# Kernel tuning notes

Hardware: AMD Instinct MI355X
Metric: run time of the kernel (lower is better)

The kernel has to match this reference:

```python
import jax, jax.numpy as jnp
import numpy as np

B = 32          # graphs per batch
NPG = 2048      # nodes per graph
N = B * NPG     # 65536 total nodes
EPG = 16384     # edges per graph
E = B * EPG     # 524288 total edges
F_IN = 129
H, C = 4, 64    # heads, per-head channels
HC = H * C      # 256
NEG_SLOPE = 0.2 # GATConv LeakyReLU slope


def setup_inputs() -> dict:
    key = jax.random.key(0)
    ks = jax.random.split(key, 20)
    # node features
    x = jax.random.normal(ks[0], (N, F_IN), dtype=jnp.float32)
    # random edges, endpoints within the same graph (per-graph contiguous node ids)
    off = (jnp.arange(B) * NPG)[:, None]
    src = (jax.random.randint(ks[1], (B, EPG), 0, NPG) + off).reshape(-1)
    dst = (jax.random.randint(ks[2], (B, EPG), 0, NPG) + off).reshape(-1)
    edge_index = jnp.stack([src, dst]).astype(jnp.int64)

    def lin(k, fan_in, shape):
        return jax.random.normal(k, shape, dtype=jnp.float32) / np.sqrt(fan_in)

    return {
        "x": x,
        "edge_index": edge_index,
        "lin0_w": lin(ks[3], F_IN, (F_IN, 256)),
        "lin0_b": jnp.zeros((256,), jnp.float32),
        "gat0_W": lin(ks[4], 256, (256, HC)),
        "gat0_asrc": lin(ks[5], C, (H, C)),
        "gat0_adst": lin(ks[6], C, (H, C)),
        "gat0_b": jnp.zeros((HC,), jnp.float32),
        "pool0_w": lin(ks[7], HC, (HC,)),
        "gat1_W": lin(ks[8], HC, (HC, HC)),
        "gat1_asrc": lin(ks[9], C, (H, C)),
        "gat1_adst": lin(ks[10], C, (H, C)),
        "gat1_b": jnp.zeros((HC,), jnp.float32),
        "pool1_w": lin(ks[11], HC, (HC,)),
        "gate_w": lin(ks[12], HC, (HC, 1)),
        "gate_b": jnp.zeros((1,), jnp.float32),
    }


def _leaky(z):
    return jnp.where(z > 0, z, NEG_SLOPE * z)


def _gat(h_in, src, dst, emask, W, asrc, adst, b):
    """PyG GATConv: shared lin, edge attention, segment softmax over dest, self-loops, concat heads."""
    n = h_in.shape[0]
    h = (h_in @ W).reshape(n, H, C)                       # [n,H,C]
    loops = jnp.arange(n)
    s = jnp.concatenate([src, loops])                     # add self loops
    d = jnp.concatenate([dst, loops])
    m = jnp.concatenate([emask, jnp.ones((n,), bool)])
    a_s = jnp.einsum('nhc,hc->nh', h, asrc)               # [n,H]
    a_d = jnp.einsum('nhc,hc->nh', h, adst)
    logit = _leaky(a_s[s] + a_d[d])                       # [E+n,H]
    logit = jnp.where(m[:, None], logit, -1e9)
    mx = jax.ops.segment_max(logit, d, num_segments=n)    # stable segment softmax
    ex = jnp.exp(logit - mx[d]) * m[:, None].astype(logit.dtype)
    den = jax.ops.segment_sum(ex, d, num_segments=n)
    coef = ex / (den[d] + 1e-16)                          # [E+n,H]
    out = jax.ops.segment_sum(h[s] * coef[:, :, None], d, num_segments=n)
    return out.reshape(n, HC) + b


def _topk_pool(hx, src, dst, emask, w, n_in, k):
    """PyG TopKPooling: score = x.w/||w||, per-graph top-k, x' = x[perm]*tanh(score[perm]), edge filter+reindex."""
    n_tot = hx.shape[0]
    bb = n_tot // n_in
    score = (hx @ w) / (jnp.linalg.norm(w) + 1e-16)       # [n_tot]
    _, idx = jax.lax.top_k(score.reshape(bb, n_in), k)    # [bb,k]
    perm = (idx + (jnp.arange(bb) * n_in)[:, None]).reshape(-1)
    xs = hx[perm] * jnp.tanh(score[perm])[:, None]
    newid = jnp.full((n_tot,), -1, jnp.int32).at[perm].set(jnp.arange(bb * k, dtype=jnp.int32))
    ns, nd = newid[src], newid[dst]
    valid = emask & (ns >= 0) & (nd >= 0)
    ns = jnp.where(valid, ns, 0)
    nd = jnp.where(valid, nd, 0)
    return xs, ns, nd, valid


def _attpool(hx, n, gate_w, gate_b):
    """AttentionalAggregation: softmax(gate_nn(x)) per graph, weighted sum."""
    bb = hx.shape[0] // n
    gate = (hx @ gate_w + gate_b).reshape(bb, n)
    wts = jax.nn.softmax(gate, axis=1)
    return jnp.einsum('bn,bnf->bf', wts, hx.reshape(bb, n, -1))


def reference(x, edge_index, lin0_w, lin0_b, gat0_W, gat0_asrc, gat0_adst, gat0_b,
              pool0_w, gat1_W, gat1_asrc, gat1_adst, gat1_b, pool1_w, gate_w, gate_b):
    src, dst = edge_index[0], edge_index[1]
    emask = jnp.ones((E,), bool)
    h = jax.nn.relu(x @ lin0_w + lin0_b)                                  # hidden MLP
    h = jax.nn.elu(_gat(h, src, dst, emask, gat0_W, gat0_asrc, gat0_adst, gat0_b))
    h, src, dst, emask = _topk_pool(h, src, dst, emask, pool0_w, NPG, NPG // 2)
    out = _attpool(h, NPG // 2, gate_w, gate_b)                           # [B,256]
    h = jax.nn.elu(_gat(h, src, dst, emask, gat1_W, gat1_asrc, gat1_adst, gat1_b))
    h, src, dst, emask = _topk_pool(h, src, dst, emask, pool1_w, NPG // 2, NPG // 4)
    out = out + _attpool(h, NPG // 4, gate_w, gate_b)
    return out
```

## Files before the change

### kernel.cpp

```cpp
#include <hip/hip_runtime.h>
#include <cmath>

namespace {

constexpr int NN0 = 65536;
constexpr int NB  = 32;
constexpr int NE  = 524288;
constexpr int EPG = 16384;
constexpr int FIN = 129;
constexpr int KP  = 160;

typedef short bf16x8 __attribute__((ext_vector_type(8)));
typedef float f32x4 __attribute__((ext_vector_type(4)));

__device__ inline float leakyrelu(float z) { return z > 0.f ? z : 0.2f * z; }
__device__ inline float eluf(float z) { return z > 0.f ? z : expm1f(z); }

__device__ inline unsigned short f2bf(float x) {
  union { float f; unsigned int u; } v; v.f = x;
  unsigned int r = v.u + 0x7fffu + ((v.u >> 16) & 1u);
  return (unsigned short)(r >> 16);
}
__device__ inline float bf2f(unsigned short h) {
  union { unsigned int u; float f; } v; v.u = ((unsigned int)h) << 16;
  return v.f;
}

__device__ inline float4 f4fma(float4 a, float c, float4 acc) {
  acc.x += a.x * c; acc.y += a.y * c; acc.z += a.z * c; acc.w += a.w * c;
  return acc;
}

__device__ inline int swz_block(int bid, int bpgl) {
  int x = bid & 7;
  int local = bid >> 3;
  int g = x + ((local >> bpgl) << 3);
  return (g << bpgl) + (local & ((1 << bpgl) - 1));
}

__device__ __forceinline__ void gload_lds16(const unsigned short* g, unsigned short* l) {
  __builtin_amdgcn_global_load_lds((const unsigned int*)g, (unsigned int*)l, 16, 0, 0);
}

__device__ inline void pack_w_body(const float* __restrict__ W, int Kreal, int idx,
                                   unsigned short* __restrict__ hi,
                                   unsigned short* __restrict__ lo) {
  int j = idx & 7;
  int lane = (idx >> 3) & 63;
  int ct = (idx >> 9) & 15;
  int kt = idx >> 13;
  int k = kt * 32 + ((lane >> 4) << 3) + j;
  int c = ct * 16 + (lane & 15);
  float v = (k < Kreal) ? W[(size_t)k * 256 + c] : 0.f;
  unsigned short h = f2bf(v);
  hi[idx] = h;
  lo[idx] = f2bf(v - bf2f(h));
}

__global__ __launch_bounds__(1024) void prep(
    const float* __restrict__ x,
    const float* __restrict__ w0, const float* __restrict__ w1,
    const float* __restrict__ w2,
    const float* __restrict__ pw0, const float* __restrict__ pw1,
    const int* __restrict__ src, const int* __restrict__ dst,
    unsigned short* __restrict__ xhi, unsigned short* __restrict__ xlo,
    unsigned short* __restrict__ whi0, unsigned short* __restrict__ wlo0,
    unsigned short* __restrict__ whi1, unsigned short* __restrict__ wlo1,
    unsigned short* __restrict__ whi2, unsigned short* __restrict__ wlo2,
    float* __restrict__ norms, int* __restrict__ newid,
    int* __restrict__ cursor, int* __restrict__ csr) {
  __shared__ int cnt[2048];
  const int NX = NN0 * KP / 8192;
  const int NW0 = 5 * 8192 / 1024;
  const int NW = 8 * 8192 / 1024;
  const int NC = NN0 / 1024;
  int b = blockIdx.x, tid = threadIdx.x;
  if (b < NX) {
    const int base = (b * 1024 + tid) * 8;
    const int row = base / KP;
    const int c0 = base - row * KP;
    const float* xr = &x[(size_t)row * FIN];
    bf16x8 hv, lv;
#pragma unroll
    for (int i = 0; i < 8; i++) {
      const int c = c0 + i;
      float v = (c < FIN) ? xr[c] : 0.f;
      unsigned short h = f2bf(v);
      hv[i] = (short)h;
      lv[i] = (short)f2bf(v - bf2f(h));
    }
    *reinterpret_cast<bf16x8*>(&xhi[base]) = hv;
    *reinterpret_cast<bf16x8*>(&xlo[base]) = lv;
    return;
  }
  b -= NX;
  if (b < NW0) { pack_w_body(w0, FIN, b * 1024 + tid, whi0, wlo0); return; }
  b -= NW0;
  if (b < NW) { pack_w_body(w1, 256, b * 1024 + tid, whi1, wlo1); return; }
  b -= NW;
  if (b < NW) { pack_w_body(w2, 256, b * 1024 + tid, whi2, wlo2); return; }
  b -= NW;
  if (b < NC) {
    newid[b * 1024 + tid] = -1;
    return;
  }
  b -= NC;
  if (b < NB) {
    const int g = b;
    cnt[tid] = 0;
    cnt[tid + 1024] = 0;
    __syncthreads();
    const int e0 = g * EPG;
    for (int i = tid; i < EPG; i += 1024) {
      int e = e0 + i;
      int d = dst[e];
      int pos = atomicAdd(&cnt[d - (g << 11)], 1);
      if (pos < 64) csr[(size_t)d * 64 + pos] = src[e];
    }
    __syncthreads();
    cursor[(g << 11) + tid] = cnt[tid];
    cursor[(g << 11) + tid + 1024] = cnt[tid + 1024];
    return;
  }
  if (tid < 64) {
    float a0 = 0.f, a1 = 0.f;
#pragma unroll
    for (int j = tid; j < 256; j += 64) {
      float v0 = pw0[j]; a0 += v0 * v0;
      float v1 = pw1[j]; a1 += v1 * v1;
    }
#pragma unroll
    for (int off = 32; off >= 1; off >>= 1) {
      a0 += __shfl_xor(a0, off);
      a1 += __shfl_xor(a1, off);
    }
    if (tid == 0) {
      norms[0] = 1.f / (sqrtf(a0) + 1e-16f);
      norms[1] = 1.f / (sqrtf(a1) + 1e-16f);
    }
  }
}

__global__ __launch_bounds__(256, 2) void gemm_fused(
    const unsigned short* __restrict__ Xhi, const unsigned short* __restrict__ Xlo,
    const unsigned short* __restrict__ B0hi, const unsigned short* __restrict__ B0lo,
    const float* __restrict__ bias0,
    const unsigned short* __restrict__ B1hi, const unsigned short* __restrict__ B1lo,
    float* __restrict__ Out,
    const float* __restrict__ attsrc, const float* __restrict__ attdst,
    float* __restrict__ a_s, float* __restrict__ a_d) {
  __shared__ __align__(16) unsigned short As[2][2][64][32];
  __shared__ __align__(16) char Hsh[2][64 * 512];
  const int tid = threadIdx.x;
  const int lane = tid & 63;
  const int w = tid >> 6;
  const int row0 = blockIdx.x * 64;
  const int l15 = lane & 15, q = lane >> 4;
  const int srow16 = lane >> 2;
  const int skc = (lane & 3) * 8;

  auto stage = [&](int nb, int kt) {
    const size_t goff = (size_t)(row0 + w * 16 + srow16) * KP + kt * 32 + skc;
    gload_lds16(Xhi + goff, &As[nb][0][w * 16][0]);
    gload_lds16(Xlo + goff, &As[nb][1][w * 16][0]);
  };

  f32x4 acc[4][4];
#pragma unroll
  for (int mf = 0; mf < 4; mf++)
#pragma unroll
    for (int nf = 0; nf < 4; nf++) acc[mf][nf] = (f32x4)(0.f);

  stage(0, 0);
  __syncthreads();

#pragma unroll
  for (int kt = 0; kt < 5; ++kt) {
    const int nb = kt & 1;
    if (kt + 1 < 5) stage(nb ^ 1, kt + 1);
    bf16x8 bh[4], bl[4];
#pragma unroll
    for (int nf = 0; nf < 4; nf++) {
      const int ct = w * 4 + nf;
      const size_t bbase = ((size_t)((kt * 16 + ct) * 64 + lane)) << 3;
      bh[nf] = *reinterpret_cast<const bf16x8*>(B0hi + bbase);
      bl[nf] = *reinterpret_cast<const bf16x8*>(B0lo + bbase);
    }
#pragma unroll
    for (int mf = 0; mf < 4; mf++) {
      const int ar = mf * 16 + l15;
      bf16x8 ah = *reinterpret_cast<const bf16x8*>(&As[nb][0][ar][q * 8]);
      bf16x8 al = *reinterpret_cast<const bf16x8*>(&As[nb][1][ar][q * 8]);
#pragma unroll
      for (int nf = 0; nf < 4; nf++) {
        acc[mf][nf] = __builtin_amdgcn_mfma_f32_16x16x32_bf16(ah, bh[nf], acc[mf][nf], 0, 0, 0);
        acc[mf][nf] = __builtin_amdgcn_mfma_f32_16x16x32_bf16(ah, bl[nf], acc[mf][nf], 0, 0, 0);
        acc[mf][nf] = __builtin_amdgcn_mfma_f32_16x16x32_bf16(al, bh[nf], acc[mf][nf], 0, 0, 0);
      }
    }
    __syncthreads();
  }

#pragma unroll
  for (int mf = 0; mf < 4; mf++) {
#pragma unroll
    for (int r = 0; r < 4; r++) {
      const int row = mf * 16 + q * 4 + r;
#pragma unroll
      for (int nf = 0; nf < 4; nf++) {
        const int col = w * 64 + nf * 16 + l15;
        float v = acc[mf][nf][r] + bias0[col];
        v = fmaxf(v, 0.f);
        unsigned short h = f2bf(v);
        unsigned short l = f2bf(v - bf2f(h));
        unsigned int off = (unsigned int)(row * 512 + col * 2) ^ ((row & 7) << 4);
        *reinterpret_cast<unsigned short*>(&Hsh[0][off]) = h;
        *reinterpret_cast<unsigned short*>(&Hsh[1][off]) = l;
        acc[mf][nf][r] = 0.f;
      }
    }
  }
  __syncthreads();

#pragma unroll
  for (int kt = 0; kt < 8; ++kt) {
    bf16x8 bh[4], bl[4];
#pragma unroll
    for (int nf = 0; nf < 4; nf++) {
      const int ct = w * 4 + nf;
      const size_t bbase = ((size_t)((kt * 16 + ct) * 64 + lane)) << 3;
      bh[nf] = *reinterpret_cast<const bf16x8*>(B1hi + bbase);
      bl[nf] = *reinterpret_cast<const bf16x8*>(B1lo + bbase);
    }
#pragma unroll
    for (int mf = 0; mf < 4; mf++) {
      const int ar = mf * 16 + l15;
      unsigned int off = (unsigned int)(ar * 512 + kt * 64 + q * 16) ^ ((ar & 7) << 4);
      bf16x8 ah = *reinterpret_cast<const bf16x8*>(&Hsh[0][off]);
      bf16x8 al = *reinterpret_cast<const bf16x8*>(&Hsh[1][off]);
#pragma unroll
      for (int nf = 0; nf < 4; nf++) {
        acc[mf][nf] = __builtin_amdgcn_mfma_f32_16x16x32_bf16(ah, bh[nf], acc[mf][nf], 0, 0, 0);
        acc[mf][nf] = __builtin_amdgcn_mfma_f32_16x16x32_bf16(ah, bl[nf], acc[mf][nf], 0, 0, 0);
        acc[mf][nf] = __builtin_amdgcn_mfma_f32_16x16x32_bf16(al, bh[nf], acc[mf][nf], 0, 0, 0);
      }
    }
  }

#pragma unroll
  for (int mf = 0; mf < 4; mf++) {
    const int rowb = row0 + mf * 16 + q * 4;
#pragma unroll
    for (int r = 0; r < 4; r++) {
#pragma unroll
      for (int nf = 0; nf < 4; nf++) {
        const int col = w * 64 + nf * 16 + l15;
        Out[(size_t)(rowb + r) * 256 + col] = acc[mf][nf][r];
      }
    }
  }
  const int head = w;
  float sv[4], dv[4];
#pragma unroll
  for (int nf = 0; nf < 4; nf++) {
    sv[nf] = attsrc[head * 64 + nf * 16 + l15];
    dv[nf] = attdst[head * 64 + nf * 16 + l15];
  }
#pragma unroll
  for (int mf = 0; mf < 4; mf++) {
#pragma unroll
    for (int r = 0; r < 4; r++) {
      float ps = 0.f, pd = 0.f;
#pragma unroll
      for (int nf = 0; nf < 4; nf++) {
        ps += acc[mf][nf][r] * sv[nf];
        pd += acc[mf][nf][r] * dv[nf];
      }
#pragma unroll
      for (int off = 8; off >= 1; off >>= 1) {
        ps += __shfl_xor(ps, off);
        pd += __shfl_xor(pd, off);
      }
      if (l15 == 0) {
        const int row = row0 + mf * 16 + q * 4 + r;
        a_s[(size_t)row * 4 + head] = ps;
        a_d[(size_t)row * 4 + head] = pd;
      }
    }
  }
}

template <int KT, bool INDIR>
__global__ __launch_bounds__(256, 2) void gemm_mfma(
    const unsigned short* __restrict__ Xhi, const unsigned short* __restrict__ Xlo,
    int ldx,
    const unsigned short* __restrict__ Bhi, const unsigned short* __restrict__ Blo,
    float* __restrict__ Out,
    const float* __restrict__ attsrc, const float* __restrict__ attdst,
    float* __restrict__ a_s, float* __restrict__ a_d,
    const int* __restrict__ rowmap, const float* __restrict__ tscale, int swzl,
    int ngemm, const float* __restrict__ partials, float* __restrict__ outp,
    int nch) {
  __shared__ __align__(16) unsigned short As[2][2][128][32];
  const int tid = threadIdx.x;
  if ((int)blockIdx.x >= ngemm) {
    int g = blockIdx.x - ngemm, c = tid;
    float a = 0.f;
    for (int s = 0; s < nch; s++) a += partials[((size_t)g * nch + s) * 256 + c];
    outp[g * 256 + c] = a;
    return;
  }
  const int lane = tid & 63;
  const int w = tid >> 6;
  const int rb = (swzl >= 0) ? swz_block(blockIdx.x, swzl) : blockIdx.x;
  const int row0 = rb * 128;
  const int l15 = lane & 15, q = lane >> 4;
  const int sl4 = lane >> 2;
  const int skc = (lane & 3) * 8;

  size_t gr[2];
#pragma unroll
  for (int i = 0; i < 2; i++) {
    int lr = row0 + (w + 4 * i) * 16 + sl4;
    gr[i] = INDIR ? (size_t)rowmap[lr] : (size_t)lr;
  }

  auto stage = [&](int nb, int kt) {
#pragma unroll
    for (int i = 0; i < 2; i++) {
      const int rbase = (w + 4 * i) * 16;
      const size_t goff = gr[i] * ldx + kt * 32 + skc;
      gload_lds16(Xhi + goff, &As[nb][0][rbase][0]);
      gload_lds16(Xlo + goff, &As[nb][1][rbase][0]);
    }
  };

  f32x4 acc[8][4];
#pragma unroll
  for (int mf = 0; mf < 8; mf++)
#pragma unroll
    for (int nf = 0; nf < 4; nf++) acc[mf][nf] = (f32x4)(0.f);

  stage(0, 0);
  __syncthreads();

#pragma unroll
  for (int kt = 0; kt < KT; ++kt) {
    const int nb = kt & 1;
    if (kt + 1 < KT) stage(nb ^ 1, kt + 1);
    bf16x8 bh[4], bl[4];
#pragma unroll
    for (int nf = 0; nf < 4; nf++) {
      const int ct = w * 4 + nf;
      const size_t bbase = ((size_t)((kt * 16 + ct) * 64 + lane)) << 3;
      bh[nf] = *reinterpret_cast<const bf16x8*>(Bhi + bbase);
      bl[nf] = *reinterpret_cast<const bf16x8*>(Blo + bbase);
    }
#pragma unroll
    for (int mf = 0; mf < 8; mf++) {
      const int ar = mf * 16 + l15;
      bf16x8 ah = *reinterpret_cast<const bf16x8*>(&As[nb][0][ar][q * 8]);
      bf16x8 al = *reinterpret_cast<const bf16x8*>(&As[nb][1][ar][q * 8]);
#pragma unroll
      for (int nf = 0; nf < 4; nf++) {
        acc[mf][nf] = __builtin_amdgcn_mfma_f32_16x16x32_bf16(ah, bh[nf], acc[mf][nf], 0, 0, 0);
        acc[mf][nf] = __builtin_amdgcn_mfma_f32_16x16x32_bf16(ah, bl[nf], acc[mf][nf], 0, 0, 0);
        acc[mf][nf] = __builtin_amdgcn_mfma_f32_16x16x32_bf16(al, bh[nf], acc[mf][nf], 0, 0, 0);
      }
    }
    __syncthreads();
  }

#pragma unroll
  for (int mf = 0; mf < 8; mf++) {
    const int rowb = row0 + mf * 16 + q * 4;
#pragma unroll
    for (int r = 0; r < 4; r++) {
      const float ts = INDIR ? tscale[rowb + r] : 1.f;
#pragma unroll
      for (int nf = 0; nf < 4; nf++) {
        float v = acc[mf][nf][r];
        if constexpr (INDIR) v *= ts;
        const int col = w * 64 + nf * 16 + l15;
        Out[(size_t)(rowb + r) * 256 + col] = v;
      }
    }
  }
  const int head = w;
  float sv[4], dv[4];
#pragma unroll
  for (int nf = 0; nf < 4; nf++) {
    sv[nf] = attsrc[head * 64 + nf * 16 + l15];
    dv[nf] = attdst[head * 64 + nf * 16 + l15];
  }
#pragma unroll
  for (int mf = 0; mf < 8; mf++) {
#pragma unroll
    for (int r = 0; r < 4; r++) {
      float ps = 0.f, pd = 0.f;
#pragma unroll
      for (int nf = 0; nf < 4; nf++) {
        ps += acc[mf][nf][r] * sv[nf];
        pd += acc[mf][nf][r] * dv[nf];
      }
#pragma unroll
      for (int off = 8; off >= 1; off >>= 1) {
        ps += __shfl_xor(ps, off);
        pd += __shfl_xor(pd, off);
      }
      if (l15 == 0) {
        const int row = row0 + mf * 16 + q * 4 + r;
        float ts = INDIR ? tscale[row] : 1.f;
        a_s[(size_t)row * 4 + head] = ps * ts;
        a_d[(size_t)row * 4 + head] = pd * ts;
      }
    }
  }
}

__global__ __launch_bounds__(256) void gat_node8(
    const int* __restrict__ cursor, const int* __restrict__ csr,
    const float* __restrict__ a_s, const float* __restrict__ a_d,
    const float* __restrict__ hW, const float* __restrict__ bias,
    const float* __restrict__ pool_w, const float* __restrict__ inv_norm,
    const float* __restrict__ gate_w,
    unsigned short* __restrict__ outHi, unsigned short* __restrict__ outLo,
    float* __restrict__ score, float* __restrict__ graw, int bpgl) {
  const int lane = threadIdx.x & 63;
  const int wv = threadIdx.x >> 6;
  const int dbase = swz_block(blockIdx.x, bpgl) * 8 + wv * 2;
  const int g = lane >> 4, l16 = lane & 15;
  const int d = dbase + (g >> 1);
  const int h0 = (g & 1) * 2;

  const int deg = min(cursor[d], 63);
  const int dim = deg + 1;

  int dmaxw = dim;
  dmaxw = max(dmaxw, __shfl_xor(dmaxw, 32));
  const int nch = (dmaxw + 15) >> 4;

  const float2 ad2 = *reinterpret_cast<const float2*>(&a_d[(size_t)d * 4 + h0]);

  int sreg[4];
  float L0[4], L1[4];
#pragma unroll
  for (int c = 0; c < 4; c++) {
    if (c < nch) {
      const int j = c * 16 + l16;
      const bool has = j < dim;
      int s = (j < deg) ? csr[(size_t)d * 64 + j] : d;
      sreg[c] = s;
      float2 as2 = *reinterpret_cast<const float2*>(&a_s[(size_t)s * 4 + h0]);
      L0[c] = has ? leakyrelu(as2.x + ad2.x) : -1e30f;
      L1[c] = has ? leakyrelu(as2.y + ad2.y) : -1e30f;
    } else {
      sreg[c] = d;
      L0[c] = -1e30f; L1[c] = -1e30f;
    }
  }
  float m0 = fmaxf(fmaxf(L0[0], L0[1]), fmaxf(L0[2], L0[3]));
  float m1 = fmaxf(fmaxf(L1[0], L1[1]), fmaxf(L1[2], L1[3]));
#pragma unroll
  for (int off = 1; off <= 8; off <<= 1) {
    m0 = fmaxf(m0, __shfl_xor(m0, off));
    m1 = fmaxf(m1, __shfl_xor(m1, off));
  }
  float e0[4], e1[4];
  float dn0 = 0.f, dn1 = 0.f;
#pragma unroll
  for (int c = 0; c < 4; c++) {
    if (c < nch) {
      e0[c] = __expf(L0[c] - m0);
      e1[c] = __expf(L1[c] - m1);
      dn0 += e0[c]; dn1 += e1[c];
    } else {
      e0[c] = 0.f; e1[c] = 0.f;
    }
  }
#pragma unroll
  for (int off = 1; off <= 8; off <<= 1) {
    dn0 += __shfl_xor(dn0, off);
    dn1 += __shfl_xor(dn1, off);
  }

  float4 acc0 = {0.f, 0.f, 0.f, 0.f}, acc1 = {0.f, 0.f, 0.f, 0.f};
#pragma unroll
  for (int c = 0; c < 4; c++) {
    if (c < nch) {
      const int tmax = min(16, dmaxw - c * 16);
#pragma unroll 2
      for (int tt = 0; tt < tmax; tt++) {
        const int idx = g * 16 + tt;
        int st = __shfl(sreg[c], idx);
        float c0 = __shfl(e0[c], idx), c1 = __shfl(e1[c], idx);
        if (c * 16 + tt < dim) {
          const float4* hp = reinterpret_cast<const float4*>(&hW[(size_t)st * 256]) + l16;
          acc0 = f4fma(hp[h0 * 16],       c0, acc0);
          acc1 = f4fma(hp[(h0 + 1) * 16], c1, acc1);
        }
      }
    }
  }

  const float iv0 = 1.f / (dn0 + 1e-16f), iv1 = 1.f / (dn1 + 1e-16f);
  float sd = 0.f, gd = 0.f;
#pragma unroll
  for (int h = 0; h < 2; h++) {
    const int coff = (h0 + h) * 64 + l16 * 4;
    float4 vb = h ? acc1 : acc0;
    float iv = h ? iv1 : iv0;
    float4 bb = *reinterpret_cast<const float4*>(&bias[coff]);
    float4 o;
    o.x = eluf(vb.x * iv + bb.x);
    o.y = eluf(vb.y * iv + bb.y);
    o.z = eluf(vb.z * iv + bb.z);
    o.w = eluf(vb.w * iv + bb.w);
    ushort4 oh, ol;
    oh.x = f2bf(o.x); ol.x = f2bf(o.x - bf2f(oh.x));
    oh.y = f2bf(o.y); ol.y = f2bf(o.y - bf2f(oh.y));
    oh.z = f2bf(o.z); ol.z = f2bf(o.z - bf2f(oh.z));
    oh.w = f2bf(o.w); ol.w = f2bf(o.w - bf2f(oh.w));
    *reinterpret_cast<ushort4*>(&outHi[(size_t)d * 256 + coff]) = oh;
    *reinterpret_cast<ushort4*>(&outLo[(size_t)d * 256 + coff]) = ol;
    float4 pw = *reinterpret_cast<const float4*>(&pool_w[coff]);
    float4 gw = *reinterpret_cast<const float4*>(&gate_w[coff]);
    sd += o.x * pw.x + o.y * pw.y + o.z * pw.z + o.w * pw.w;
    gd += o.x * gw.x + o.y * gw.y + o.z * gw.z + o.w * gw.w;
  }
#pragma unroll
  for (int off = 1; off <= 16; off <<= 1) {
    sd += __shfl_xor(sd, off);
    gd += __shfl_xor(gd, off);
  }
  if ((lane & 31) == 0) {
    score[d] = sd * inv_norm[0];
    graw[d] = gd;
  }
}

__global__ __launch_bounds__(1024) void topk_hsel(
    const float* __restrict__ score, const float* __restrict__ graw,
    const float* __restrict__ gate_b, int npg, int k,
    int* __restrict__ perm, int* __restrict__ newid,
    float* __restrict__ gate, float* __restrict__ tsc) {
  __shared__ unsigned keys[2048];
  __shared__ int hist[1024];
  __shared__ int ssum[1024];
  __shared__ int segtot[16];
  __shared__ unsigned wmin[16], wmax[16];
  __shared__ int sstate[3];
  __shared__ int scnt;
  __shared__ int candi[512];
  __shared__ unsigned candk[512];
  __shared__ float fred[1024];
  const int g = blockIdx.x, tid = threadIdx.x;
  const int wv = tid >> 6, ln = tid & 63;
  const size_t base = (size_t)g * npg;

  unsigned mymin = 0xFFFFFFFFu, mymax = 0u;
  for (int i = tid; i < npg; i += 1024) {
    unsigned u = __float_as_uint(score[base + i]);
    u = (u & 0x80000000u) ? ~u : (u | 0x80000000u);
    keys[i] = u;
    mymin = min(mymin, u);
    mymax = max(mymax, u);
  }
#pragma unroll
  for (int off = 32; off >= 1; off >>= 1) {
    mymin = min(mymin, (unsigned)__shfl_xor((int)mymin, off));
    mymax = max(mymax, (unsigned)__shfl_xor((int)mymax, off));
  }
  if (ln == 0) { wmin[wv] = mymin; wmax[wv] = mymax; }
  __syncthreads();
  unsigned lo, hi;
  {
    unsigned a = 0xFFFFFFFFu, b = 0u;
#pragma unroll
    for (int i = 0; i < 16; i++) { a = min(a, wmin[i]); b = max(b, wmax[i]); }
    lo = a; hi = b;
  }
  int need = k;

  for (int iter = 0; iter < 4; ++iter) {
    unsigned long long range = (unsigned long long)(hi - lo) + 1ull;
    unsigned width = (unsigned)((range + 1023ull) >> 10);
    hist[tid] = 0;
    __syncthreads();
    for (int i = tid; i < npg; i += 1024) {
      unsigned u = keys[i];
      if (u >= lo && u <= hi) atomicAdd(&hist[(u - lo) / width], 1);
    }
    __syncthreads();
    int v = hist[tid];
    int s = v;
#pragma unroll
    for (int off = 1; off < 64; off <<= 1) {
      int t = __shfl_down(s, off);
      if (ln + off < 64) s += t;
    }
    if (ln == 0) segtot[wv] = s;
    __syncthreads();
    if (tid == 0) {
      int acc = 0;
      for (int i = 15; i >= 0; i--) { int t = segtot[i]; segtot[i] = acc; acc += t; }
    }
    __syncthreads();
    int S = s + segtot[wv];
    ssum[tid] = S;
    __syncthreads();
    int gt = (tid == 1023) ? 0 : ssum[tid + 1];
    if (S >= need && gt < need) {
      sstate[0] = tid;
      sstate[1] = gt;
      sstate[2] = hist[tid];
    }
    __syncthreads();
    const int bstar = sstate[0], cntAbove = sstate[1], m = sstate[2];
    unsigned nlo = lo + (unsigned)bstar * width;
    unsigned long long nhiu = (unsigned long long)lo + (unsigned long long)(bstar + 1) * width - 1ull;
    unsigned nhi = (nhiu > (unsigned long long)hi) ? hi : (unsigned)nhiu;
    need -= cntAbove;
    lo = nlo; hi = nhi;
    __syncthreads();
    if (width == 1 || m <= 256) break;
  }

  if (tid == 0) scnt = 0;
  __syncthreads();
  for (int i = tid; i < npg; i += 1024) {
    unsigned u = keys[i];
    if (u >= lo && u <= hi) {
      int pidx = atomicAdd(&scnt, 1);
      if (pidx < 512) { candi[pidx] = i; candk[pidx] = u; }
    }
  }
  __syncthreads();
  const int m_all = scnt;
  const float gb = gate_b[0];
  if (tid == 0) scnt = 0;
  __syncthreads();
  for (int i = tid; i < npg; i += 1024) {
    if (keys[i] > hi) {
      int pos = atomicAdd(&scnt, 1);
      int node = (int)(base + i);
      perm[g * k + pos] = node;
      if (newid) newid[node] = g * k + pos;
      float ts = tanhf(score[base + i]);
      tsc[g * k + pos] = ts;
      gate[g * k + pos] = ts * graw[node] + gb;
    }
  }
  __syncthreads();
  const int nAbove = scnt;
  if (m_all <= 512) {
    for (int c = tid; c < m_all; c += 1024) {
      unsigned u = candk[c];
      int i = candi[c];
      int rank = 0;
      for (int j = 0; j < m_all; j++) {
        unsigned vk = candk[j];
        rank += (vk > u) || (vk == u && candi[j] < i);
      }
      if (rank < need) {
        int pos = nAbove + rank;
        int node = (int)(base + i);
        perm[g * k + pos] = node;
        if (newid) newid[node] = g * k + pos;
        float ts = tanhf(score[base + i]);
        tsc[g * k + pos] = ts;
        gate[g * k + pos] = ts * graw[node] + gb;
      }
    }
  } else {
    for (int i = tid; i < npg; i += 1024) {
      unsigned u = keys[i];
      if (u >= lo && u <= hi) {
        int rank = 0;
        for (int j = 0; j < npg; j++) {
          unsigned vk = keys[j];
          if (vk >= lo && vk <= hi) rank += (vk > u) || (vk == u && j < i);
        }
        if (rank < need) {
          int pos = nAbove + rank;
          int node = (int)(base + i);
          perm[g * k + pos] = node;
          if (newid) newid[node] = g * k + pos;
          float ts = tanhf(score[base + i]);
          tsc[g * k + pos] = ts;
          gate[g * k + pos] = ts * graw[node] + gb;
        }
      }
    }
  }
  __syncthreads();

  float gv = (tid < k) ? gate[g * k + tid] : -1e30f;
  fred[tid] = gv;
  __syncthreads();
  for (int s = 512; s >= 1; s >>= 1) {
    if (tid < s) fred[tid] = fmaxf(fred[tid], fred[tid + s]);
    __syncthreads();
  }
  const float gm = fred[0];
  __syncthreads();
  float ge = (tid < k) ? __expf(gv - gm) : 0.f;
  fred[tid] = ge;
  __syncthreads();
  for (int s = 512; s >= 1; s >>= 1) {
    if (tid < s) fred[tid] += fred[tid + s];
    __syncthreads();
  }
  const float ginv = 1.f / fred[0];
  if (tid < k) gate[g * k + tid] = ge * ginv * tsc[g * k + tid];
}

__global__ __launch_bounds__(1024) void pool_tail(
    const unsigned short* __restrict__ xhi, const unsigned short* __restrict__ xlo,
    const int* __restrict__ perm, const float* __restrict__ wfin,
    float* __restrict__ partials, int npg, int bpgl, int nsum,
    const int* __restrict__ src, const int* __restrict__ dst,
    const int* __restrict__ newid, int* __restrict__ cursor2,
    int* __restrict__ csr, int do_scatter) {
  __shared__ int cnt[1024];
  const int tid = threadIdx.x;
  if ((int)blockIdx.x < nsum) {
    int o = swz_block(blockIdx.x, bpgl);
    int g = o >> bpgl, lb = o & ((1 << bpgl) - 1);
    int part = tid >> 8, c = tid & 255;
    int sub = lb * 4 + part;
    size_t r0 = (size_t)g * npg + sub * 32;
    float a = 0.f;
#pragma unroll 8
    for (int i = 0; i < 32; i++) {
      float wv = wfin[r0 + i];
      size_t node = (size_t)perm[r0 + i];
      float v = bf2f(xhi[node * 256 + c]) + bf2f(xlo[node * 256 + c]);
      a += wv * v;
    }
    partials[((size_t)g * (npg >> 5) + sub) * 256 + c] = a;
    return;
  }
  if (!do_scatter) return;
  const int g = blockIdx.x - nsum;
  cnt[tid] = 0;
  __syncthreads();
  const int e0 = g * EPG;
  for (int i = tid; i < EPG; i += 1024) {
    int e = e0 + i;
    int s = newid[src[e]], d = newid[dst[e]];
    if (s < 0 || d < 0) continue;
    int pos = atomicAdd(&cnt[d - (g << 10)], 1);
    if (pos < 64) csr[(size_t)d * 64 + pos] = s;
  }
  __syncthreads();
  cursor2[(g << 10) + tid] = cnt[tid];
}

__global__ __launch_bounds__(256) void attpool_reduce(const float* __restrict__ partials,
                                                      float* __restrict__ out,
                                                      int nch, int acc_flag) {
  int g = blockIdx.x, c = threadIdx.x;
  float a = 0.f;
  for (int s = 0; s < nch; s++) a += partials[((size_t)g * nch + s) * 256 + c];
  if (acc_flag) out[g * 256 + c] += a;
  else out[g * 256 + c] = a;
}

}

extern "C" void kernel_launch(void* const* d_in, const int* in_sizes, int n_in,
                              void* d_out, int out_size, void* d_ws, size_t ws_size,
                              hipStream_t stream) {
  (void)in_sizes; (void)n_in; (void)out_size; (void)ws_size;
  const float* x       = (const float*)d_in[0];
  const int*   ei      = (const int*)d_in[1];
  const float* lin0_w  = (const float*)d_in[2];
  const float* lin0_b  = (const float*)d_in[3];
  const float* gat0_W  = (const float*)d_in[4];
  const float* gat0_as = (const float*)d_in[5];
  const float* gat0_ad = (const float*)d_in[6];
  const float* gat0_b  = (const float*)d_in[7];
  const float* pool0_w = (const float*)d_in[8];
  const float* gat1_W  = (const float*)d_in[9];
  const float* gat1_as = (const float*)d_in[10];
  const float* gat1_ad = (const float*)d_in[11];
  const float* gat1_b  = (const float*)d_in[12];
  const float* pool1_w = (const float*)d_in[13];
  const float* gate_w  = (const float*)d_in[14];
  const float* gate_b  = (const float*)d_in[15];
  float* out = (float*)d_out;
  const int* srcp = ei;
  const int* dstp = ei + NE;

  char* wsb = (char*)d_ws;
  size_t cur = 0;
  auto alloc = [&](size_t bytes) {
    void* p = wsb + cur;
    cur = (cur + bytes + 255) & ~(size_t)255;
    return p;
  };
  char* regA = (char*)alloc((size_t)NN0 * 256 * 4);
  char* regB = (char*)alloc((size_t)NN0 * 256 * 4);
  char* regD = (char*)alloc((size_t)NN0 * KP * 2 * 2);
  float* a_s     = (float*)alloc((size_t)NN0 * 4 * 4);
  float* a_d     = (float*)alloc((size_t)NN0 * 4 * 4);
  int*   cursor  = (int*)alloc((size_t)NN0 * 4);
  int*   cursor2 = (int*)alloc((size_t)32768 * 4);
  int*   csr     = (int*)alloc((size_t)NN0 * 64 * 4);
  float* score   = (float*)alloc((size_t)NN0 * 4);
  float* graw    = (float*)alloc((size_t)NN0 * 4);
  int*   newid   = (int*)alloc((size_t)NN0 * 4);
  int*   perm0   = (int*)alloc((size_t)32768 * 4);
  int*   perm1   = (int*)alloc((size_t)16384 * 4);
  float* tsc0    = (float*)alloc((size_t)32768 * 4);
  float* tsc1    = (float*)alloc((size_t)16384 * 4);
  float* gate0   = (float*)alloc((size_t)32768 * 4);
  float* gate1   = (float*)alloc((size_t)16384 * 4);
  float* partials= (float*)alloc((size_t)NB * 32 * 256 * 4);
  float* norms   = (float*)alloc(2 * 4);
  unsigned short* whi0 = (unsigned short*)alloc((size_t)5 * 8192 * 2);
  unsigned short* wlo0 = (unsigned short*)alloc((size_t)5 * 8192 * 2);
  unsigned short* whi1 = (unsigned short*)alloc((size_t)8 * 8192 * 2);
  unsigned short* wlo1 = (unsigned short*)alloc((size_t)8 * 8192 * 2);
  unsigned short* whi2 = (unsigned short*)alloc((size_t)8 * 8192 * 2);
  unsigned short* wlo2 = (unsigned short*)alloc((size_t)8 * 8192 * 2);

  unsigned short* xhi = (unsigned short*)regD;
  unsigned short* xlo = xhi + (size_t)NN0 * KP;
  float* hW0  = (float*)regB;
  unsigned short* out0hi = (unsigned short*)regA;
  unsigned short* out0lo = out0hi + (size_t)NN0 * 256;
  float* hW1  = (float*)regB;
  unsigned short* out1hi = (unsigned short*)(regB + (size_t)32768 * 256 * 4);
  unsigned short* out1lo = out1hi + (size_t)32768 * 256;

  {
    int grid = NN0 * KP / 8192 + 40 + 64 + 64 + 64 + NB + 1;
    prep<<<grid, 1024, 0, stream>>>(x, lin0_w, gat0_W, gat1_W, pool0_w, pool1_w,
                                    srcp, dstp,
                                    xhi, xlo, whi0, wlo0, whi1, wlo1, whi2, wlo2,
                                    norms, newid, cursor, csr);
  }

  gemm_fused<<<NN0 / 64, 256, 0, stream>>>(
      xhi, xlo, whi0, wlo0, lin0_b, whi1, wlo1, hW0,
      gat0_as, gat0_ad, a_s, a_d);

  gat_node8<<<NN0 / 8, 256, 0, stream>>>(cursor, csr, a_s, a_d, hW0,
                                         gat0_b, pool0_w, norms, gate_w,
                                         out0hi, out0lo, score, graw, 8);

  topk_hsel<<<NB, 1024, 0, stream>>>(score, graw, gate_b, 2048, 1024,
                                     perm0, newid, gate0, tsc0);
  pool_tail<<<NB * 8 + NB, 1024, 0, stream>>>(out0hi, out0lo, perm0, gate0,
                                              partials, 1024, 3, NB * 8,
                                              srcp, dstp, newid, cursor2, csr, 1);

  gemm_mfma<8, true><<<32768 / 128 + NB, 256, 0, stream>>>(
      out0hi, out0lo, 256, whi2, wlo2, hW1,
      gat1_as, gat1_ad, a_s, a_d, perm0, tsc0, 3,
      32768 / 128, partials, out, 32);

  gat_node8<<<32768 / 8, 256, 0, stream>>>(cursor2, csr, a_s, a_d, hW1,
                                           gat1_b, pool1_w, norms + 1, gate_w,
                                           out1hi, out1lo, score, graw, 7);

  topk_hsel<<<NB, 1024, 0, stream>>>(score, graw, gate_b, 1024, 512,
                                     perm1, nullptr, gate1, tsc1);
  pool_tail<<<NB * 4, 1024, 0, stream>>>(out1hi, out1lo, perm1, gate1,
                                         partials, 512, 2, NB * 4,
                                         nullptr, nullptr, nullptr, nullptr,
                                         nullptr, 0);
  attpool_reduce<<<NB, 256, 0, stream>>>(partials, out, 16, 1);
}
```

Baseline: 263.6 us.

## Split per-graph CSR build across eight blocks using global atomic base offsets

The per-graph edge bucketing in prep and pool_tail, which ran as one block per graph over 16384 edges, is split into 8 slice blocks per graph. Each slice counts its destinations in LDS, reserves a range with global atomics on a cursor that is now zeroed by memset, then scatters its sources. The scatter blocks are placed first in the grid so these long-running blocks start early. This adds two memset launches, a second pass over the edges, and global atomics, and it makes the order of neighbors in each CSR row nondeterministic.

After: 253.5 us. 3.8% less time.

```diff
diff --git a/kernel.cpp b/kernel.cpp
--- a/kernel.cpp
+++ b/kernel.cpp
@@ -57,6 +57,8 @@
   lo[idx] = f2bf(v - bf2f(h));
 }
 
+constexpr int SLC = 8;
+
 __global__ __launch_bounds__(1024) void prep(
     const float* __restrict__ x,
     const float* __restrict__ w0, const float* __restrict__ w1,
@@ -70,11 +72,39 @@
     float* __restrict__ norms, int* __restrict__ newid,
     int* __restrict__ cursor, int* __restrict__ csr) {
   __shared__ int cnt[2048];
+  __shared__ int basev[2048];
+  const int NSC = NB * SLC;
   const int NX = NN0 * KP / 8192;
   const int NW0 = 5 * 8192 / 1024;
   const int NW = 8 * 8192 / 1024;
   const int NC = NN0 / 1024;
   int b = blockIdx.x, tid = threadIdx.x;
+  if (b < NSC) {
+    const int g = b / SLC, sl = b % SLC;
+    const int e0 = g * EPG + sl * (EPG / SLC);
+    const int ne = EPG / SLC;
+    cnt[tid] = 0; cnt[tid + 1024] = 0;
+    __syncthreads();
+    for (int i = tid; i < ne; i += 1024)
+      atomicAdd(&cnt[dst[e0 + i] - (g << 11)], 1);
+    __syncthreads();
+    for (int k = tid; k < 2048; k += 1024) {
+      int c = cnt[k];
+      basev[k] = c ? atomicAdd(&cursor[(g << 11) + k], c) : 0;
+    }
+    __syncthreads();
+    cnt[tid] = 0; cnt[tid + 1024] = 0;
+    __syncthreads();
+    for (int i = tid; i < ne; i += 1024) {
+      int e = e0 + i;
+      int d = dst[e];
+      int lb = d - (g << 11);
+      int pos = basev[lb] + atomicAdd(&cnt[lb], 1);
+      if (pos < 64) csr[(size_t)d * 64 + pos] = src[e];
+    }
+    return;
+  }
+  b -= NSC;
   if (b < NX) {
     const int base = (b * 1024 + tid) * 8;
     const int row = base / KP;
@@ -102,24 +132,6 @@
   b -= NW;
   if (b < NC) {
     newid[b * 1024 + tid] = -1;
-    return;
-  }
-  b -= NC;
-  if (b < NB) {
-    const int g = b;
-    cnt[tid] = 0;
-    cnt[tid + 1024] = 0;
-    __syncthreads();
-    const int e0 = g * EPG;
-    for (int i = tid; i < EPG; i += 1024) {
-      int e = e0 + i;
-      int d = dst[e];
-      int pos = atomicAdd(&cnt[d - (g << 11)], 1);
-      if (pos < 64) csr[(size_t)d * 64 + pos] = src[e];
-    }
-    __syncthreads();
-    cursor[(g << 11) + tid] = cnt[tid];
-    cursor[(g << 11) + tid + 1024] = cnt[tid + 1024];
     return;
   }
   if (tid < 64) {
@@ -718,43 +730,57 @@
 __global__ __launch_bounds__(1024) void pool_tail(
     const unsigned short* __restrict__ xhi, const unsigned short* __restrict__ xlo,
     const int* __restrict__ perm, const float* __restrict__ wfin,
-    float* __restrict__ partials, int npg, int bpgl, int nsum,
+    float* __restrict__ partials, int npg, int bpgl, int nsc,
     const int* __restrict__ src, const int* __restrict__ dst,
     const int* __restrict__ newid, int* __restrict__ cursor2,
-    int* __restrict__ csr, int do_scatter) {
+    int* __restrict__ csr) {
   __shared__ int cnt[1024];
+  __shared__ int basev[1024];
   const int tid = threadIdx.x;
-  if ((int)blockIdx.x < nsum) {
-    int o = swz_block(blockIdx.x, bpgl);
-    int g = o >> bpgl, lb = o & ((1 << bpgl) - 1);
-    int part = tid >> 8, c = tid & 255;
-    int sub = lb * 4 + part;
-    size_t r0 = (size_t)g * npg + sub * 32;
-    float a = 0.f;
+  if ((int)blockIdx.x < nsc) {
+    const int g = blockIdx.x / SLC, sl = blockIdx.x % SLC;
+    const int e0 = g * EPG + sl * (EPG / SLC);
+    const int ne = EPG / SLC;
+    cnt[tid] = 0;
+    __syncthreads();
+    for (int i = tid; i < ne; i += 1024) {
+      int e = e0 + i;
+      int s = newid[src[e]], d = newid[dst[e]];
+      if (s >= 0 && d >= 0) atomicAdd(&cnt[d - (g << 10)], 1);
+    }
+    __syncthreads();
+    {
+      int c = cnt[tid];
+      basev[tid] = c ? atomicAdd(&cursor2[(g << 10) + tid], c) : 0;
+    }
+    __syncthreads();
+    cnt[tid] = 0;
+    __syncthreads();
+    for (int i = tid; i < ne; i += 1024) {
+      int e = e0 + i;
+      int s = newid[src[e]], d = newid[dst[e]];
+      if (s < 0 || d < 0) continue;
+      int lb = d - (g << 10);
+      int pos = basev[lb] + atomicAdd(&cnt[lb], 1);
+      if (pos < 64) csr[(size_t)d * 64 + pos] = s;
+    }
+    return;
+  }
+  int rel = blockIdx.x - nsc;
+  int o = swz_block(rel, bpgl);
+  int g = o >> bpgl, lb = o & ((1 << bpgl) - 1);
+  int part = tid >> 8, c = tid & 255;
+  int sub = lb * 4 + part;
+  size_t r0 = (size_t)g * npg + sub * 32;
+  float a = 0.f;
 #pragma unroll 8
-    for (int i = 0; i < 32; i++) {
-      float wv = wfin[r0 + i];
-      size_t node = (size_t)perm[r0 + i];
-      float v = bf2f(xhi[node * 256 + c]) + bf2f(xlo[node * 256 + c]);
-      a += wv * v;
-    }
-    partials[((size_t)g * (npg >> 5) + sub) * 256 + c] = a;
-    return;
-  }
-  if (!do_scatter) return;
-  const int g = blockIdx.x - nsum;
-  cnt[tid] = 0;
-  __syncthreads();
-  const int e0 = g * EPG;
-  for (int i = tid; i < EPG; i += 1024) {
-    int e = e0 + i;
-    int s = newid[src[e]], d = newid[dst[e]];
-    if (s < 0 || d < 0) continue;
-    int pos = atomicAdd(&cnt[d - (g << 10)], 1);
-    if (pos < 64) csr[(size_t)d * 64 + pos] = s;
-  }
-  __syncthreads();
-  cursor2[(g << 10) + tid] = cnt[tid];
+  for (int i = 0; i < 32; i++) {
+    float wv = wfin[r0 + i];
+    size_t node = (size_t)perm[r0 + i];
+    float v = bf2f(xhi[node * 256 + c]) + bf2f(xlo[node * 256 + c]);
+    a += wv * v;
+  }
+  partials[((size_t)g * (npg >> 5) + sub) * 256 + c] = a;
 }
 
 __global__ __launch_bounds__(256) void attpool_reduce(const float* __restrict__ partials,
@@ -835,8 +861,11 @@
   unsigned short* out1hi = (unsigned short*)(regB + (size_t)32768 * 256 * 4);
   unsigned short* out1lo = out1hi + (size_t)32768 * 256;
 
+  hipMemsetAsync(cursor, 0, (size_t)NN0 * 4, stream);
+  hipMemsetAsync(cursor2, 0, (size_t)32768 * 4, stream);
+
   {
-    int grid = NN0 * KP / 8192 + 40 + 64 + 64 + 64 + NB + 1;
+    int grid = NB * SLC + NN0 * KP / 8192 + 40 + 64 + 64 + 64 + 1;
     prep<<<grid, 1024, 0, stream>>>(x, lin0_w, gat0_W, gat1_W, pool0_w, pool1_w,
                                     srcp, dstp,
                                     xhi, xlo, whi0, wlo0, whi1, wlo1, whi2, wlo2,
@@ -853,9 +882,9 @@
 
   topk_hsel<<<NB, 1024, 0, stream>>>(score, graw, gate_b, 2048, 1024,
                                      perm0, newid, gate0, tsc0);
-  pool_tail<<<NB * 8 + NB, 1024, 0, stream>>>(out0hi, out0lo, perm0, gate0,
-                                              partials, 1024, 3, NB * 8,
-                                              srcp, dstp, newid, cursor2, csr, 1);
+  pool_tail<<<NB * SLC + NB * 8, 1024, 0, stream>>>(
+      out0hi, out0lo, perm0, gate0, partials, 1024, 3, NB * SLC,
+      srcp, dstp, newid, cursor2, csr);
 
   gemm_mfma<8, true><<<32768 / 128 + NB, 256, 0, stream>>>(
       out0hi, out0lo, 256, whi2, wlo2, hW1,
@@ -868,9 +897,8 @@
 
   topk_hsel<<<NB, 1024, 0, stream>>>(score, graw, gate_b, 1024, 512,
                                      perm1, nullptr, gate1, tsc1);
-  pool_tail<<<NB * 4, 1024, 0, stream>>>(out1hi, out1lo, perm1, gate1,
-                                         partials, 512, 2, NB * 4,
-                                         nullptr, nullptr, nullptr, nullptr,
-                                         nullptr, 0);
+  pool_tail<<<NB * 4, 1024, 0, stream>>>(
+      out1hi, out1lo, perm1, gate1, partials, 512, 2, 0,
+      nullptr, nullptr, nullptr, nullptr, nullptr);
   attpool_reduce<<<NB, 256, 0, stream>>>(partials, out, 16, 1);
 }
```
